# Kernel tuning notes

Measured on AMD Instinct MI355X. Metric: run time of the kernel, lower is better.

Reference implementation:

```python
import jax, jax.numpy as jnp
import numpy as np

NUM_NODES = 100000   # rows of data.x
D = 512              # embedding dim (data.x.shape[1]); include_senses=False so input dim == D
H = 1024             # n_units
V = 50000            # last_idx_globals - last_idx_senses
B, T = 4, 512


def setup_inputs() -> dict:
    key = jax.random.key(0)
    ks = jax.random.split(key, 10)
    s = 0.02
    return {
        "token_idx": jax.random.randint(ks[0], (B, T), 0, 75000),
        "X": jax.random.normal(ks[1], (NUM_NODES, D), jnp.float32) * s,
        # LSTM layer 0: input D -> hidden H ; gate order i,f,g,o (torch convention)
        "W_ih0": jax.random.normal(ks[2], (4 * H, D), jnp.float32) * s,
        "W_hh0": jax.random.normal(ks[3], (4 * H, H), jnp.float32) * s,
        "b0": jnp.zeros((4 * H,), jnp.float32),
        # LSTM layer 1: H -> H
        "W_ih1": jax.random.normal(ks[4], (4 * H, H), jnp.float32) * s,
        "W_hh1": jax.random.normal(ks[5], (4 * H, H), jnp.float32) * s,
        "b1": jnp.zeros((4 * H,), jnp.float32),
        # linear2global
        "W_out": jax.random.normal(ks[6], (V, H), jnp.float32) * s,
        "b_out": jnp.zeros((V,), jnp.float32),
    }


def _lstm_layer(x, Wih, Whh, b):
    # x: [B, T, in] -> hidden sequence [B, T, H]
    Bq = x.shape[0]
    Hh = Whh.shape[1]
    # input contribution for all timesteps at once (one big GEMM)
    xg = jnp.einsum('bti,gi->btg', x, Wih) + b  # [B, T, 4H]

    def step(carry, xt):
        h, c = carry
        g = xt + h @ Whh.T  # [B, 4H]
        i, f, gg, o = jnp.split(g, 4, axis=-1)
        i = jax.nn.sigmoid(i); f = jax.nn.sigmoid(f)
        gg = jnp.tanh(gg); o = jax.nn.sigmoid(o)
        c = f * c + i * gg
        h = o * jnp.tanh(c)
        return (h, c), h

    h0 = jnp.zeros((Bq, Hh), x.dtype)
    (_, _), hs = jax.lax.scan(step, (h0, h0), jnp.swapaxes(xg, 0, 1))
    return jnp.swapaxes(hs, 0, 1)  # [B, T, H]


def reference(token_idx, X, W_ih0, W_hh0, b0, W_ih1, W_hh1, b1, W_out, b_out):
    emb = X[token_idx]                 # embedding gather: [B, T, D]
    h = _lstm_layer(emb, W_ih0, W_hh0, b0)
    h = _lstm_layer(h, W_ih1, W_hh1, b1)
    logits = jnp.einsum('bth,vh->btv', h, W_out) + b_out  # linear2global
    return jax.nn.log_softmax(logits, axis=-1)            # [B, T, V]
```

## Files before the change

### kernel.cpp

```cpp
#include <hip/hip_runtime.h>
#include <stdint.h>

#define B_ 4
#define T_ 512
#define D_ 512
#define H_ 1024
#define V_ 50000
#define VPAD 50048
#define M_ (B_*T_)
#define G4 (4*H_)

typedef __attribute__((ext_vector_type(8))) short bf16x8;
typedef __attribute__((ext_vector_type(4))) float f32x4;

__device__ __forceinline__ ushort f2bf(float f){
  uint32_t u = __float_as_uint(f);
  u += 0x7fffu + ((u >> 16) & 1u);
  return (ushort)(u >> 16);
}

__global__ void cvt4_kernel(const float* __restrict__ src, ushort* __restrict__ dst,
                            int n4_src, int n4_dst){
  int i = blockIdx.x * blockDim.x + threadIdx.x;
  if (i >= n4_dst) return;
  ushort4 r; r.x = 0; r.y = 0; r.z = 0; r.w = 0;
  if (i < n4_src){
    float4 v = reinterpret_cast<const float4*>(src)[i];
    r.x = f2bf(v.x); r.y = f2bf(v.y); r.z = f2bf(v.z); r.w = f2bf(v.w);
  }
  reinterpret_cast<ushort4*>(dst)[i] = r;
}

__global__ void gather_kernel(const int* __restrict__ idx, const float* __restrict__ X,
                              ushort* __restrict__ emb){
  int row = blockIdx.x;
  int tok = idx[row];
  const float* src = X + (size_t)tok * D_;
  ushort* dst = emb + (size_t)row * D_;
  for (int k = threadIdx.x; k < D_; k += blockDim.x) dst[k] = f2bf(src[k]);
}

__global__ __launch_bounds__(256) void gemm_kernel(
    const ushort* __restrict__ A, const ushort* __restrict__ Bm,
    const float* __restrict__ bias, float* __restrict__ C,
    int K, int Nreal, int ldc){
  __shared__ ushort As[128*64];
  __shared__ ushort Bs[128*64];
  const int tid = threadIdx.x;
  const int w = tid >> 6, l = tid & 63;
  const int tm = blockIdx.y, tn = blockIdx.x;
  const int wm = (w >> 1) * 64, wn = (w & 1) * 64;
  const int lq = l & 15, quad = l >> 4;

  f32x4 acc[4][4];
  #pragma unroll
  for (int i = 0; i < 4; i++)
    #pragma unroll
    for (int j = 0; j < 4; j++) acc[i][j] = (f32x4){0.f,0.f,0.f,0.f};

  const int srow = l >> 3;
  const int sg   = (l & 7) ^ srow;

  for (int kt = 0; kt < K; kt += 64){
    #pragma unroll
    for (int q = 0; q < 4; q++){
      const int iss = w*4 + q;
      const int row = iss*8 + srow;
      const ushort* ga = A  + (size_t)(tm*128 + row)*K + kt + sg*8;
      const ushort* gb = Bm + (size_t)(tn*128 + row)*K + kt + sg*8;
      __builtin_amdgcn_global_load_lds((const __attribute__((address_space(1))) void*)ga,
          (__attribute__((address_space(3))) void*)(&As[iss*512]), 16, 0, 0);
      __builtin_amdgcn_global_load_lds((const __attribute__((address_space(1))) void*)gb,
          (__attribute__((address_space(3))) void*)(&Bs[iss*512]), 16, 0, 0);
    }
    __syncthreads();
    #pragma unroll
    for (int kc = 0; kc < 2; kc++){
      bf16x8 af[4], bf[4];
      const int G = kc*4 + quad;
      #pragma unroll
      for (int i = 0; i < 4; i++){
        int rowA = wm + i*16 + lq;
        af[i] = *reinterpret_cast<const bf16x8*>(&As[rowA*64 + (G ^ (rowA & 7))*8]);
        int rowB = wn + i*16 + lq;
        bf[i] = *reinterpret_cast<const bf16x8*>(&Bs[rowB*64 + (G ^ (rowB & 7))*8]);
      }
      #pragma unroll
      for (int i = 0; i < 4; i++)
        #pragma unroll
        for (int j = 0; j < 4; j++)
          acc[i][j] = __builtin_amdgcn_mfma_f32_16x16x32_bf16(af[i], bf[j], acc[i][j], 0, 0, 0);
    }
    __syncthreads();
  }
  #pragma unroll
  for (int j = 0; j < 4; j++){
    int col = tn*128 + wn + j*16 + lq;
    bool ok = col < Nreal;
    float bv = ok ? bias[col] : 0.f;
    #pragma unroll
    for (int i = 0; i < 4; i++){
      int row0 = tm*128 + wm + i*16 + quad*4;
      #pragma unroll
      for (int r = 0; r < 4; r++){
        if (ok) C[(size_t)(row0 + r)*ldc + col] = acc[i][j][r] + bv;
      }
    }
  }
}

__global__ __launch_bounds__(256, 1) void lstm_step_kernel(
    const ushort* __restrict__ Whh,
    const float*  __restrict__ xg,
    const ushort* __restrict__ h_in,
    ushort* __restrict__ h_out,
    float*  __restrict__ c_buf,
    ushort* __restrict__ hseq,
    int t){
  const int tid = threadIdx.x;
  const int w = tid >> 6, l = tid & 63;
  const int wg = blockIdx.x;
  const int lq = l & 15, quad = l >> 4;
  __shared__ float gates[4][4][16];

  const ushort* wp = Whh + (size_t)(w*H_ + wg*16 + lq)*H_ + quad*8;
  const ushort* ap = h_in + (size_t)(lq & 3)*H_ + quad*8;

  bf16x8 bfr[32], afr[32];
  #pragma unroll
  for (int c = 0; c < 32; c++) bfr[c] = *reinterpret_cast<const bf16x8*>(wp + c*32);
  #pragma unroll
  for (int c = 0; c < 32; c++) afr[c] = *reinterpret_cast<const bf16x8*>(ap + c*32);
  f32x4 acc = (f32x4){0.f,0.f,0.f,0.f};
  #pragma unroll
  for (int c = 0; c < 32; c++)
    acc = __builtin_amdgcn_mfma_f32_16x16x32_bf16(afr[c], bfr[c], acc, 0, 0, 0);

  if (l < 16){
    #pragma unroll
    for (int r = 0; r < 4; r++) gates[w][r][l] = acc[r];
  }
  __syncthreads();
  if (tid < 64){
    const int b = tid >> 4, j = tid & 15;
    const int jj = wg*16 + j;
    const size_t xbase = ((size_t)b*T_ + t)*G4;
    float pi = gates[0][b][j] + xg[xbase + 0*H_ + jj];
    float pf = gates[1][b][j] + xg[xbase + 1*H_ + jj];
    float pg = gates[2][b][j] + xg[xbase + 2*H_ + jj];
    float po = gates[3][b][j] + xg[xbase + 3*H_ + jj];
    float ig = 1.f/(1.f + __expf(-pi));
    float fg = 1.f/(1.f + __expf(-pf));
    float gv = tanhf(pg);
    float og = 1.f/(1.f + __expf(-po));
    float c  = fg * c_buf[b*H_ + jj] + ig * gv;
    c_buf[b*H_ + jj] = c;
    float h  = og * tanhf(c);
    ushort hb = f2bf(h);
    h_out[b*H_ + jj] = hb;
    hseq[((size_t)b*T_ + t)*H_ + jj] = hb;
  }
}

__global__ void lse_kernel(const float* __restrict__ out, float* __restrict__ rowlse){
  int row = blockIdx.x;
  const float* p = out + (size_t)row * V_;
  float s = 0.f;
  for (int k = threadIdx.x; k < V_; k += blockDim.x) s += __expf(p[k]);
  #pragma unroll
  for (int off = 32; off > 0; off >>= 1) s += __shfl_down(s, off);
  __shared__ float red[4];
  if ((threadIdx.x & 63) == 0) red[threadIdx.x >> 6] = s;
  __syncthreads();
  if (threadIdx.x == 0) rowlse[row] = logf(red[0] + red[1] + red[2] + red[3]);
}

__global__ void apply_kernel(float* __restrict__ out, const float* __restrict__ rowlse){
  int row = blockIdx.y;
  int xi = blockIdx.x * blockDim.x + threadIdx.x;
  if (xi >= V_/4) return;
  float4* p = reinterpret_cast<float4*>(out + (size_t)row * V_);
  float ls = rowlse[row];
  float4 v = p[xi];
  v.x -= ls; v.y -= ls; v.z -= ls; v.w -= ls;
  p[xi] = v;
}

extern "C" void kernel_launch(void* const* d_in, const int* in_sizes, int n_in,
                              void* d_out, int out_size, void* d_ws, size_t ws_size,
                              hipStream_t stream){
  const int*   idx   = (const int*)  d_in[0];
  const float* X     = (const float*)d_in[1];
  const float* Wih0  = (const float*)d_in[2];
  const float* Whh0  = (const float*)d_in[3];
  const float* b0    = (const float*)d_in[4];
  const float* Wih1  = (const float*)d_in[5];
  const float* Whh1  = (const float*)d_in[6];
  const float* b1    = (const float*)d_in[7];
  const float* Wout  = (const float*)d_in[8];
  const float* bout  = (const float*)d_in[9];
  float* out = (float*)d_out;

  char* ws = (char*)d_ws;
  size_t off = 0;
  auto alloc = [&](size_t bytes){ void* p = ws + off; off = (off + bytes + 255) & ~(size_t)255; return p; };
  ushort* emb   = (ushort*)alloc((size_t)M_*D_*2);
  ushort* wih0b = (ushort*)alloc((size_t)G4*D_*2);
  ushort* whh0b = (ushort*)alloc((size_t)G4*H_*2);
  ushort* wih1b = (ushort*)alloc((size_t)G4*H_*2);
  ushort* whh1b = (ushort*)alloc((size_t)G4*H_*2);
  ushort* woutb = (ushort*)alloc((size_t)VPAD*H_*2);
  float*  xgbuf = (float*)alloc((size_t)M_*G4*4);
  ushort* h0seq = (ushort*)alloc((size_t)M_*H_*2);
  ushort* h1seq = (ushort*)alloc((size_t)M_*H_*2);
  ushort* hb0   = (ushort*)alloc(2*(size_t)B_*H_*2);
  float*  cb0   = (float*) alloc((size_t)B_*H_*4);
  ushort* hb1   = (ushort*)alloc(2*(size_t)B_*H_*2);
  float*  cb1   = (float*) alloc((size_t)B_*H_*4);
  float*  rowlse= (float*) alloc((size_t)M_*4);

  {
    int n4;
    n4 = G4*D_/4; cvt4_kernel<<<(n4+255)/256, 256, 0, stream>>>(Wih0, wih0b, n4, n4);
    n4 = G4*H_/4; cvt4_kernel<<<(n4+255)/256, 256, 0, stream>>>(Whh0, whh0b, n4, n4);
    n4 = G4*H_/4; cvt4_kernel<<<(n4+255)/256, 256, 0, stream>>>(Wih1, wih1b, n4, n4);
    n4 = G4*H_/4; cvt4_kernel<<<(n4+255)/256, 256, 0, stream>>>(Whh1, whh1b, n4, n4);
    int n4d = VPAD*H_/4, n4s = V_*H_/4;
    cvt4_kernel<<<(n4d+255)/256, 256, 0, stream>>>(Wout, woutb, n4s, n4d);
  }
  gather_kernel<<<M_, 256, 0, stream>>>(idx, X, emb);

  hipMemsetAsync(hb0, 0, 2*(size_t)B_*H_*2, stream);
  hipMemsetAsync(cb0, 0, (size_t)B_*H_*4, stream);
  hipMemsetAsync(hb1, 0, 2*(size_t)B_*H_*2, stream);
  hipMemsetAsync(cb1, 0, (size_t)B_*H_*4, stream);

  gemm_kernel<<<dim3(G4/128, M_/128), 256, 0, stream>>>(emb, wih0b, b0, xgbuf, D_, G4, G4);
  for (int t = 0; t < T_; t++)
    lstm_step_kernel<<<64, 256, 0, stream>>>(whh0b, xgbuf,
        hb0 + (size_t)(t&1)*B_*H_, hb0 + (size_t)((t+1)&1)*B_*H_, cb0, h0seq, t);

  gemm_kernel<<<dim3(G4/128, M_/128), 256, 0, stream>>>(h0seq, wih1b, b1, xgbuf, H_, G4, G4);
  for (int t = 0; t < T_; t++)
    lstm_step_kernel<<<64, 256, 0, stream>>>(whh1b, xgbuf,
        hb1 + (size_t)(t&1)*B_*H_, hb1 + (size_t)((t+1)&1)*B_*H_, cb1, h1seq, t);

  gemm_kernel<<<dim3(VPAD/128, M_/128), 256, 0, stream>>>(h1seq, woutb, bout, out, H_, V_, V_);
  lse_kernel<<<M_, 256, 0, stream>>>(out, rowlse);
  apply_kernel<<<dim3((V_/4+255)/256, M_), 256, 0, stream>>>(out, rowlse);
}
```

Before: 11.16 ms.

## Replace per-timestep LSTM launches with persistent kernel using grid barrier

The 512 per-timestep launches for each LSTM layer are replaced by one persistent kernel per layer. Each block keeps its slice of W_hh in registers for all timesteps and holds the cell state in a register. Blocks synchronise between steps with an atomic-counter grid barrier, and the next step's xg values are prefetched. The MFMA chain is also split across two accumulators for more ILP. This removes launch overhead and repeated weight reloads, but it relies on all 64 blocks being co-resident and adds the latency of a spin barrier.

Result: faster. 9.393 ms (-15.8%).

```diff
diff --git a/kernel.cpp b/kernel.cpp
--- a/kernel.cpp
+++ b/kernel.cpp
@@ -76,20 +76,20 @@
     __syncthreads();
     #pragma unroll
     for (int kc = 0; kc < 2; kc++){
-      bf16x8 af[4], bf[4];
+      bf16x8 af[4], bfv[4];
       const int G = kc*4 + quad;
       #pragma unroll
       for (int i = 0; i < 4; i++){
         int rowA = wm + i*16 + lq;
         af[i] = *reinterpret_cast<const bf16x8*>(&As[rowA*64 + (G ^ (rowA & 7))*8]);
         int rowB = wn + i*16 + lq;
-        bf[i] = *reinterpret_cast<const bf16x8*>(&Bs[rowB*64 + (G ^ (rowB & 7))*8]);
+        bfv[i] = *reinterpret_cast<const bf16x8*>(&Bs[rowB*64 + (G ^ (rowB & 7))*8]);
       }
       #pragma unroll
       for (int i = 0; i < 4; i++)
         #pragma unroll
         for (int j = 0; j < 4; j++)
-          acc[i][j] = __builtin_amdgcn_mfma_f32_16x16x32_bf16(af[i], bf[j], acc[i][j], 0, 0, 0);
+          acc[i][j] = __builtin_amdgcn_mfma_f32_16x16x32_bf16(af[i], bfv[j], acc[i][j], 0, 0, 0);
     }
     __syncthreads();
   }
@@ -109,14 +109,12 @@
   }
 }
 
-__global__ __launch_bounds__(256, 1) void lstm_step_kernel(
+__global__ __launch_bounds__(256, 1) void lstm_persist_kernel(
     const ushort* __restrict__ Whh,
     const float*  __restrict__ xg,
-    const ushort* __restrict__ h_in,
-    ushort* __restrict__ h_out,
-    float*  __restrict__ c_buf,
+    ushort* __restrict__ hbuf,
     ushort* __restrict__ hseq,
-    int t){
+    unsigned int* __restrict__ barcnt){
   const int tid = threadIdx.x;
   const int w = tid >> 6, l = tid & 63;
   const int wg = blockIdx.x;
@@ -124,41 +122,76 @@
   __shared__ float gates[4][4][16];
 
   const ushort* wp = Whh + (size_t)(w*H_ + wg*16 + lq)*H_ + quad*8;
-  const ushort* ap = h_in + (size_t)(lq & 3)*H_ + quad*8;
-
-  bf16x8 bfr[32], afr[32];
+  bf16x8 bfr[32];
   #pragma unroll
   for (int c = 0; c < 32; c++) bfr[c] = *reinterpret_cast<const bf16x8*>(wp + c*32);
-  #pragma unroll
-  for (int c = 0; c < 32; c++) afr[c] = *reinterpret_cast<const bf16x8*>(ap + c*32);
-  f32x4 acc = (f32x4){0.f,0.f,0.f,0.f};
-  #pragma unroll
-  for (int c = 0; c < 32; c++)
-    acc = __builtin_amdgcn_mfma_f32_16x16x32_bf16(afr[c], bfr[c], acc, 0, 0, 0);
-
-  if (l < 16){
-    #pragma unroll
-    for (int r = 0; r < 4; r++) gates[w][r][l] = acc[r];
-  }
-  __syncthreads();
-  if (tid < 64){
-    const int b = tid >> 4, j = tid & 15;
-    const int jj = wg*16 + j;
-    const size_t xbase = ((size_t)b*T_ + t)*G4;
-    float pi = gates[0][b][j] + xg[xbase + 0*H_ + jj];
-    float pf = gates[1][b][j] + xg[xbase + 1*H_ + jj];
-    float pg = gates[2][b][j] + xg[xbase + 2*H_ + jj];
-    float po = gates[3][b][j] + xg[xbase + 3*H_ + jj];
-    float ig = 1.f/(1.f + __expf(-pi));
-    float fg = 1.f/(1.f + __expf(-pf));
-    float gv = tanhf(pg);
-    float og = 1.f/(1.f + __expf(-po));
-    float c  = fg * c_buf[b*H_ + jj] + ig * gv;
-    c_buf[b*H_ + jj] = c;
-    float h  = og * tanhf(c);
-    ushort hb = f2bf(h);
-    h_out[b*H_ + jj] = hb;
-    hseq[((size_t)b*T_ + t)*H_ + jj] = hb;
+
+  const int gb = tid >> 4, gj = tid & 15;
+  const int jj = wg*16 + gj;
+  const bool gm = (tid < 64);
+  float creg = 0.f;
+
+  float xv0 = 0.f, xv1 = 0.f, xv2 = 0.f, xv3 = 0.f;
+  if (gm){
+    const size_t xb = ((size_t)gb*T_ + 0)*G4 + jj;
+    xv0 = xg[xb];        xv1 = xg[xb + H_];
+    xv2 = xg[xb + 2*H_]; xv3 = xg[xb + 3*H_];
+  }
+  const unsigned int nwg = gridDim.x;
+
+  for (int t = 0; t < T_; t++){
+    const ushort* hin  = hbuf + (size_t)(t & 1)*(B_*H_);
+    ushort*       hout = hbuf + (size_t)((t + 1) & 1)*(B_*H_);
+    const ushort* ap = hin + (size_t)(lq & 3)*H_ + quad*8;
+
+    f32x4 acc0 = (f32x4){0.f,0.f,0.f,0.f};
+    f32x4 acc1 = (f32x4){0.f,0.f,0.f,0.f};
+    #pragma unroll
+    for (int cc = 0; cc < 4; cc++){
+      bf16x8 a[8];
+      #pragma unroll
+      for (int c = 0; c < 8; c++) a[c] = *reinterpret_cast<const bf16x8*>(ap + (cc*8 + c)*32);
+      #pragma unroll
+      for (int c = 0; c < 4; c++){
+        acc0 = __builtin_amdgcn_mfma_f32_16x16x32_bf16(a[2*c],   bfr[cc*8 + 2*c],   acc0, 0, 0, 0);
+        acc1 = __builtin_amdgcn_mfma_f32_16x16x32_bf16(a[2*c+1], bfr[cc*8 + 2*c+1], acc1, 0, 0, 0);
+      }
+    }
+    if (l < 16){
+      #pragma unroll
+      for (int r = 0; r < 4; r++) gates[w][r][l] = acc0[r] + acc1[r];
+    }
+    __syncthreads();
+    if (gm){
+      float pi = gates[0][gb][gj] + xv0;
+      float pf = gates[1][gb][gj] + xv1;
+      float pg = gates[2][gb][gj] + xv2;
+      float po = gates[3][gb][gj] + xv3;
+      float ig = 1.f/(1.f + __expf(-pi));
+      float fg = 1.f/(1.f + __expf(-pf));
+      float gv = tanhf(pg);
+      float og = 1.f/(1.f + __expf(-po));
+      creg = fg * creg + ig * gv;
+      float h  = og * tanhf(creg);
+      ushort hb = f2bf(h);
+      hout[gb*H_ + jj] = hb;
+      hseq[((size_t)gb*T_ + t)*H_ + jj] = hb;
+      if (t + 1 < T_){
+        const size_t xb = ((size_t)gb*T_ + (t + 1))*G4 + jj;
+        xv0 = xg[xb];        xv1 = xg[xb + H_];
+        xv2 = xg[xb + 2*H_]; xv3 = xg[xb + 3*H_];
+      }
+    }
+    __syncthreads();
+    if (tid == 0){
+      __threadfence();
+      __hip_atomic_fetch_add(barcnt, 1u, __ATOMIC_RELAXED, __HIP_MEMORY_SCOPE_AGENT);
+      const unsigned int tgt = (unsigned int)(t + 1) * nwg;
+      while (__hip_atomic_load(barcnt, __ATOMIC_RELAXED, __HIP_MEMORY_SCOPE_AGENT) < tgt)
+        __builtin_amdgcn_s_sleep(1);
+      __threadfence();
+    }
+    __syncthreads();
   }
 }
 
@@ -214,10 +247,9 @@
   ushort* h0seq = (ushort*)alloc((size_t)M_*H_*2);
   ushort* h1seq = (ushort*)alloc((size_t)M_*H_*2);
   ushort* hb0   = (ushort*)alloc(2*(size_t)B_*H_*2);
-  float*  cb0   = (float*) alloc((size_t)B_*H_*4);
   ushort* hb1   = (ushort*)alloc(2*(size_t)B_*H_*2);
-  float*  cb1   = (float*) alloc((size_t)B_*H_*4);
   float*  rowlse= (float*) alloc((size_t)M_*4);
+  unsigned int* bar = (unsigned int*)alloc(256);
 
   {
     int n4;
@@ -231,19 +263,14 @@
   gather_kernel<<<M_, 256, 0, stream>>>(idx, X, emb);
 
   hipMemsetAsync(hb0, 0, 2*(size_t)B_*H_*2, stream);
-  hipMemsetAsync(cb0, 0, (size_t)B_*H_*4, stream);
   hipMemsetAsync(hb1, 0, 2*(size_t)B_*H_*2, stream);
-  hipMemsetAsync(cb1, 0, (size_t)B_*H_*4, stream);
+  hipMemsetAsync(bar, 0, 256, stream);
 
   gemm_kernel<<<dim3(G4/128, M_/128), 256, 0, stream>>>(emb, wih0b, b0, xgbuf, D_, G4, G4);
-  for (int t = 0; t < T_; t++)
-    lstm_step_kernel<<<64, 256, 0, stream>>>(whh0b, xgbuf,
-        hb0 + (size_t)(t&1)*B_*H_, hb0 + (size_t)((t+1)&1)*B_*H_, cb0, h0seq, t);
+  lstm_persist_kernel<<<64, 256, 0, stream>>>(whh0b, xgbuf, hb0, h0seq, bar + 0);
 
   gemm_kernel<<<dim3(G4/128, M_/128), 256, 0, stream>>>(h0seq, wih1b, b1, xgbuf, H_, G4, G4);
-  for (int t = 0; t < T_; t++)
-    lstm_step_kernel<<<64, 256, 0, stream>>>(whh1b, xgbuf,
-        hb1 + (size_t)(t&1)*B_*H_, hb1 + (size_t)((t+1)&1)*B_*H_, cb1, h1seq, t);
+  lstm_persist_kernel<<<64, 256, 0, stream>>>(whh1b, xgbuf, hb1, h1seq, bar + 64);
 
   gemm_kernel<<<dim3(VPAD/128, M_/128), 256, 0, stream>>>(h1seq, woutb, bout, out, H_, V_, V_);
   lse_kernel<<<M_, 256, 0, stream>>>(out, rowlse);
```
